# Kernel tuning notes

Hardware: AMD Instinct MI355X
Metric: run time of the kernel (lower is better)

The kernel has to match this reference:

```python
import jax, jax.numpy as jnp
import numpy as np

N_SPK, N_UTT, D = 1024, 32, 128
EPS = 1e-8  # matches F.cosine_similarity eps


def setup_inputs() -> dict:
    key = jax.random.key(0)
    emb = jax.random.normal(key, (N_SPK * N_UTT, D), dtype=jnp.float32)
    emb = emb / jnp.linalg.norm(emb, axis=-1, keepdims=True)  # L2-normalized per docstring
    return {
        "embeddings": emb,
        "w": jnp.asarray(10.0, dtype=jnp.float32),
        "b": jnp.asarray(-5.0, dtype=jnp.float32),
        "n_speakers": N_SPK,
        "n_utterances": N_UTT,
    }


def reference(embeddings, w, b, n_speakers, n_utterances):
    # [N, M, D]
    e = embeddings.reshape(n_speakers, n_utterances, -1)
    cent = e.mean(axis=1)  # [N, D] full centroids
    # exclusive centroids: mean over all utterances except i -> [N, M, D]
    cent_excl = (e.sum(axis=1, keepdims=True) - e) / (n_utterances - 1)

    e_n = jnp.maximum(jnp.linalg.norm(e, axis=-1), EPS)          # [N, M]
    c_n = jnp.maximum(jnp.linalg.norm(cent, axis=-1), EPS)       # [N]
    ce_n = jnp.maximum(jnp.linalg.norm(cent_excl, axis=-1), EPS) # [N, M]

    # cosine sim of every utterance vs every full centroid: [N, M, N]
    sim = jnp.einsum('nmd,kd->nmk', e, cent) / (e_n[:, :, None] * c_n[None, None, :])
    # own-speaker entry uses the exclusive centroid instead
    sim_own = jnp.sum(e * cent_excl, axis=-1) / (e_n * ce_n)     # [N, M]
    eye = jnp.eye(n_speakers, dtype=bool)[:, None, :]            # [N, 1, N]
    sim = jnp.where(eye, sim_own[:, :, None], sim)

    logits = (w * sim + b).reshape(n_speakers * n_utterances, n_speakers)
    targets = jnp.repeat(jnp.arange(n_speakers), n_utterances)
    logp = jax.nn.log_softmax(logits, axis=-1)
    loss = -jnp.take_along_axis(logp, targets[:, None], axis=-1).mean()
    return loss
```

## Files before the change

kernel.cpp:

```cpp
#include <hip/hip_runtime.h>
#include <math.h>

#define NSPK 1024
#define NUTT 32
#define DIM  128
#define NROWS (NSPK * NUTT)
#define EPS 1e-8f
#define LOG2E 1.44269504f

typedef __attribute__((ext_vector_type(8))) short short8;
typedef __attribute__((ext_vector_type(4))) float floatx4;

__device__ inline unsigned short f2bf(float f) {
  union { float f; unsigned u; } v; v.f = f;
  unsigned r = v.u + 0x7fffu + ((v.u >> 16) & 1u);
  return (unsigned short)(r >> 16);
}

__global__ __launch_bounds__(256) void k1(const float* __restrict__ emb,
                                          const float* __restrict__ wp,
                                          const float* __restrict__ bp,
                                          unsigned short* __restrict__ centN,
                                          float* __restrict__ rs2g,
                                          float* __restrict__ eolg,
                                          float* __restrict__ olvg,
                                          float* __restrict__ out) {
  __shared__ __align__(16) float Sl[2 * 128];
  __shared__ float red[4];

  int b = blockIdx.x, t = threadIdx.x;
  float w = wp[0], bb = bp[0];
  float M = bb + fabsf(w);
  if (b == 0 && t == 0) out[0] = 0.f;

  int sp = t >> 7, d = t & 127;
  {
    const float* eb = emb + (size_t)(b * 2 + sp) * NUTT * DIM + d;
    float s = 0.f;
#pragma unroll
    for (int m = 0; m < NUTT; ++m) s += eb[m * DIM];
    Sl[sp * 128 + d] = s;
    float p = s * s;
#pragma unroll
    for (int mask = 1; mask < 64; mask <<= 1) p += __shfl_xor(p, mask, 64);
    if ((t & 63) == 0) red[t >> 6] = p;
  }
  __syncthreads();
  float ss0 = red[0] + red[1], ss1 = red[2] + red[3];

  {
    float ss = sp ? ss1 : ss0;
    float s = Sl[sp * 128 + d];
    float cn = fmaxf(sqrtf(ss) * (1.0f / NUTT), EPS);
    centN[(size_t)(b * 2 + sp) * DIM + d] = f2bf(s / (NUTT * cn));
  }

  {
    int row = t >> 2, sub = t & 3;
    int rsp = row >> 5;
    const float* er = emb + (size_t)(b * 64 + row) * DIM + sub * 32;
    const float* Srow = &Sl[rsp * 128 + sub * 32];
    float ee = 0.f, es = 0.f;
#pragma unroll
    for (int i = 0; i < 8; ++i) {
      float4 ev = *(const float4*)&er[i * 4];
      float4 sv = *(const float4*)&Srow[i * 4];
      ee += ev.x * ev.x + ev.y * ev.y + ev.z * ev.z + ev.w * ev.w;
      es += ev.x * sv.x + ev.y * sv.y + ev.z * sv.z + ev.w * sv.w;
    }
    ee += __shfl_xor(ee, 1, 64); es += __shfl_xor(es, 1, 64);
    ee += __shfl_xor(ee, 2, 64); es += __shfl_xor(es, 2, 64);
    if (sub == 0) {
      float ss = rsp ? ss1 : ss0;
      float en = fmaxf(sqrtf(ee), EPS);
      float dot_own = (es - ee) * (1.0f / (NUTT - 1));
      float ex2 = (ss - 2.f * es + ee) * (1.0f / ((NUTT - 1) * (NUTT - 1)));
      float cen = fmaxf(sqrtf(ex2), EPS);
      float ol = w * dot_own / (en * cen) + bb;
      int gr = b * 64 + row;
      olvg[gr] = ol;
      eolg[gr] = exp2f((ol - M) * LOG2E);
      rs2g[gr] = w * LOG2E / en;
    }
  }
}

__global__ __launch_bounds__(256, 2) void k2(const float* __restrict__ emb,
                                             const unsigned short* __restrict__ centN,
                                             const float* __restrict__ rs2g,
                                             const float* __restrict__ eolg,
                                             const float* __restrict__ olvg,
                                             const float* __restrict__ wp,
                                             const float* __restrict__ bp,
                                             float* __restrict__ out) {
  __shared__ __align__(16) unsigned short A[64 * 136];
  __shared__ __align__(16) unsigned short Bb[2][64 * 136];
  __shared__ __align__(16) float sPart[256];

  int b = blockIdx.x, t = threadIdx.x;
  float w = wp[0], bb = bp[0];
  float M = bb + fabsf(w);
  float c2 = -fabsf(w) * LOG2E;

#pragma unroll
  for (int i = 0; i < 8; ++i) {
    int idx4 = t + 256 * i;
    int r = idx4 >> 5, d4 = (idx4 & 31) << 2;
    float4 v = *(const float4*)(emb + (size_t)b * 8192 + (size_t)idx4 * 4);
    ushort4 bv;
    bv.x = f2bf(v.x); bv.y = f2bf(v.y); bv.z = f2bf(v.z); bv.w = f2bf(v.w);
    *(ushort4*)&A[r * 136 + d4] = bv;
  }
  __syncthreads();

  int wid = t >> 6, lane = t & 63, lg = lane >> 4, lc = lane & 15;

  short8 af[4][4];
#pragma unroll
  for (int rt = 0; rt < 4; ++rt)
#pragma unroll
    for (int ks = 0; ks < 4; ++ks)
      af[rt][ks] = *(const short8*)&A[(rt * 16 + lc) * 136 + ks * 32 + lg * 8];

  float rsL[16], eolL[16];
#pragma unroll
  for (int rt = 0; rt < 4; ++rt) {
    float4 r4 = *(const float4*)&rs2g[b * 64 + rt * 16 + lg * 4];
    float4 o4 = *(const float4*)&eolg[b * 64 + rt * 16 + lg * 4];
    rsL[rt * 4 + 0] = r4.x; rsL[rt * 4 + 1] = r4.y; rsL[rt * 4 + 2] = r4.z; rsL[rt * 4 + 3] = r4.w;
    eolL[rt * 4 + 0] = o4.x; eolL[rt * 4 + 1] = o4.y; eolL[rt * 4 + 2] = o4.z; eolL[rt * 4 + 3] = o4.w;
  }

  float sAcc[16];
#pragma unroll
  for (int j = 0; j < 16; ++j) sAcc[j] = 0.f;

  short8 R[4];
#pragma unroll
  for (int i = 0; i < 4; ++i) {
    int f = t + 256 * i;
    R[i] = *(const short8*)(centN + (size_t)(f >> 4) * DIM + (f & 15) * 8);
  }

  for (int p = 0; p < 16; ++p) {
    unsigned short* Bp = Bb[p & 1];
    __syncthreads();
#pragma unroll
    for (int i = 0; i < 4; ++i) {
      int f = t + 256 * i;
      *(short8*)&Bp[(f >> 4) * 136 + (f & 15) * 8] = R[i];
    }
    {
      int pn = (p + 1) & 15;
#pragma unroll
      for (int i = 0; i < 4; ++i) {
        int f = t + 256 * i;
        R[i] = *(const short8*)(centN + (size_t)(pn * 64 + (f >> 4)) * DIM + (f & 15) * 8);
      }
    }
    __syncthreads();

    short8 bf[4];
#pragma unroll
    for (int ks = 0; ks < 4; ++ks)
      bf[ks] = *(const short8*)&Bp[(wid * 16 + lc) * 136 + ks * 32 + lg * 8];

    floatx4 acc[4];
#pragma unroll
    for (int rt = 0; rt < 4; ++rt) acc[rt] = (floatx4){0.f, 0.f, 0.f, 0.f};
#pragma unroll
    for (int ks = 0; ks < 4; ++ks)
#pragma unroll
      for (int rt = 0; rt < 4; ++rt)
        acc[rt] = __builtin_amdgcn_mfma_f32_16x16x32_bf16(af[rt][ks], bf[ks], acc[rt], 0, 0, 0);

    int col = p * 64 + wid * 16 + lc;
#pragma unroll
    for (int rt = 0; rt < 4; ++rt) {
      int own = b * 2 + (rt >> 1);
      bool isown = (col == own);
#pragma unroll
      for (int reg = 0; reg < 4; ++reg) {
        float l2 = fmaf(rsL[rt * 4 + reg], acc[rt][reg], c2);
        float e = exp2f(l2);
        if (isown) e = eolL[rt * 4 + reg];
        sAcc[rt * 4 + reg] += e;
      }
    }
  }

#pragma unroll
  for (int mask = 1; mask < 16; mask <<= 1)
#pragma unroll
    for (int j = 0; j < 16; ++j) sAcc[j] += __shfl_xor(sAcc[j], mask, 64);

  if (lc == 0)
#pragma unroll
    for (int rt = 0; rt < 4; ++rt)
#pragma unroll
      for (int reg = 0; reg < 4; ++reg)
        sPart[wid * 64 + rt * 16 + lg * 4 + reg] = sAcc[rt * 4 + reg];
  __syncthreads();

  if (t < 64) {
    float st = sPart[t] + sPart[64 + t] + sPart[128 + t] + sPart[192 + t];
    float lossr = M + logf(st) - olvg[b * 64 + t];
#pragma unroll
    for (int mask = 1; mask < 64; mask <<= 1) lossr += __shfl_xor(lossr, mask, 64);
    if (t == 0) atomicAdd(out, lossr * (1.0f / NROWS));
  }
}

extern "C" void kernel_launch(void* const* d_in, const int* in_sizes, int n_in,
                              void* d_out, int out_size, void* d_ws, size_t ws_size,
                              hipStream_t stream) {
  const float* emb = (const float*)d_in[0];
  const float* wp  = (const float*)d_in[1];
  const float* bp  = (const float*)d_in[2];

  char* ws = (char*)d_ws;
  unsigned short* centN = (unsigned short*)ws;
  float* rs2g = (float*)(ws + 262144);
  float* eolg = (float*)(ws + 262144 + 131072);
  float* olvg = (float*)(ws + 262144 + 262144);
  float* out = (float*)d_out;

  hipLaunchKernelGGL(k1, dim3(512), dim3(256), 0, stream,
                     emb, wp, bp, centN, rs2g, eolg, olvg, out);
  hipLaunchKernelGGL(k2, dim3(512), dim3(256), 0, stream,
                     emb, centN, rs2g, eolg, olvg, wp, bp, out);
}
```

Before: 93.81 us.

## Stream centroid tiles straight into LDS with global_load_lds and a chunked layout

k1 now writes the normalized bf16 centroids in a layout grouped into 8-element chunks along the feature dimension. k2 loads each 64-centroid tile with asynchronous global-to-LDS loads (global_load_lds) instead of staging through registers and copying into padded shared memory. Each lane's MFMA B-fragment read becomes one contiguous, conflict-free 16-byte LDS access, and one barrier per iteration is removed. The cost is that correctness now depends on the barrier waiting for the asynchronous LDS writes to finish, and the centroid layout is more specialized.

```diff
diff --git a/kernel.cpp b/kernel.cpp
--- a/kernel.cpp
+++ b/kernel.cpp
@@ -17,10 +17,16 @@
   return (unsigned short)(r >> 16);
 }
 
+__device__ __forceinline__ void gll16(const unsigned short* g, unsigned short* l) {
+  __builtin_amdgcn_global_load_lds(
+      (const __attribute__((address_space(1))) unsigned int*)g,
+      (__attribute__((address_space(3))) unsigned int*)l, 16, 0, 0);
+}
+
 __global__ __launch_bounds__(256) void k1(const float* __restrict__ emb,
                                           const float* __restrict__ wp,
                                           const float* __restrict__ bp,
-                                          unsigned short* __restrict__ centN,
+                                          unsigned short* __restrict__ centC,
                                           float* __restrict__ rs2g,
                                           float* __restrict__ eolg,
                                           float* __restrict__ olvg,
@@ -52,7 +58,8 @@
     float ss = sp ? ss1 : ss0;
     float s = Sl[sp * 128 + d];
     float cn = fmaxf(sqrtf(ss) * (1.0f / NUTT), EPS);
-    centN[(size_t)(b * 2 + sp) * DIM + d] = f2bf(s / (NUTT * cn));
+    centC[(size_t)(d >> 3) * (NSPK * 8) + (size_t)(b * 2 + sp) * 8 + (d & 7)] =
+        f2bf(s / (NUTT * cn));
   }
 
   {
@@ -86,7 +93,7 @@
 }
 
 __global__ __launch_bounds__(256, 2) void k2(const float* __restrict__ emb,
-                                             const unsigned short* __restrict__ centN,
+                                             const unsigned short* __restrict__ centC,
                                              const float* __restrict__ rs2g,
                                              const float* __restrict__ eolg,
                                              const float* __restrict__ olvg,
@@ -94,10 +101,11 @@
                                              const float* __restrict__ bp,
                                              float* __restrict__ out) {
   __shared__ __align__(16) unsigned short A[64 * 136];
-  __shared__ __align__(16) unsigned short Bb[2][64 * 136];
+  __shared__ __align__(16) unsigned short Bb[2][8192];
   __shared__ __align__(16) float sPart[256];
 
   int b = blockIdx.x, t = threadIdx.x;
+  int wid = t >> 6, lane = t & 63, lg = lane >> 4, lc = lane & 15;
   float w = wp[0], bb = bp[0];
   float M = bb + fabsf(w);
   float c2 = -fabsf(w) * LOG2E;
@@ -111,9 +119,15 @@
     bv.x = f2bf(v.x); bv.y = f2bf(v.y); bv.z = f2bf(v.z); bv.w = f2bf(v.w);
     *(ushort4*)&A[r * 136 + d4] = bv;
   }
+
+  const unsigned short* gbase = centC + ((size_t)(wid * 4 + lg) * NSPK + lc) * 8;
+  {
+#pragma unroll
+    for (int i = 0; i < 4; ++i)
+      gll16(gbase + (size_t)i * 16 * 8, &Bb[0][i * 2048 + wid * 512]);
+  }
+
   __syncthreads();
-
-  int wid = t >> 6, lane = t & 63, lg = lane >> 4, lc = lane & 15;
 
   short8 af[4][4];
 #pragma unroll
@@ -135,35 +149,21 @@
 #pragma unroll
   for (int j = 0; j < 16; ++j) sAcc[j] = 0.f;
 
-  short8 R[4];
-#pragma unroll
-  for (int i = 0; i < 4; ++i) {
-    int f = t + 256 * i;
-    R[i] = *(const short8*)(centN + (size_t)(f >> 4) * DIM + (f & 15) * 8);
-  }
-
   for (int p = 0; p < 16; ++p) {
-    unsigned short* Bp = Bb[p & 1];
-    __syncthreads();
-#pragma unroll
-    for (int i = 0; i < 4; ++i) {
-      int f = t + 256 * i;
-      *(short8*)&Bp[(f >> 4) * 136 + (f & 15) * 8] = R[i];
-    }
-    {
-      int pn = (p + 1) & 15;
-#pragma unroll
-      for (int i = 0; i < 4; ++i) {
-        int f = t + 256 * i;
-        R[i] = *(const short8*)(centN + (size_t)(pn * 64 + (f >> 4)) * DIM + (f & 15) * 8);
-      }
-    }
-    __syncthreads();
-
+    if (p > 0) __syncthreads();
+    if (p < 15) {
+      const unsigned short* gp = gbase + (size_t)(p + 1) * 64 * 8;
+      unsigned short* lb = Bb[(p + 1) & 1];
+#pragma unroll
+      for (int i = 0; i < 4; ++i)
+        gll16(gp + (size_t)i * 16 * 8, &lb[i * 2048 + wid * 512]);
+    }
+
+    const unsigned short* Bp = Bb[p & 1];
     short8 bf[4];
 #pragma unroll
     for (int ks = 0; ks < 4; ++ks)
-      bf[ks] = *(const short8*)&Bp[(wid * 16 + lc) * 136 + ks * 32 + lg * 8];
+      bf[ks] = *(const short8*)&Bp[wid * 2048 + ks * 512 + lane * 8];
 
     floatx4 acc[4];
 #pragma unroll
@@ -219,14 +219,14 @@
   const float* bp  = (const float*)d_in[2];
 
   char* ws = (char*)d_ws;
-  unsigned short* centN = (unsigned short*)ws;
+  unsigned short* centC = (unsigned short*)ws;
   float* rs2g = (float*)(ws + 262144);
   float* eolg = (float*)(ws + 262144 + 131072);
   float* olvg = (float*)(ws + 262144 + 262144);
   float* out = (float*)d_out;
 
   hipLaunchKernelGGL(k1, dim3(512), dim3(256), 0, stream,
-                     emb, wp, bp, centN, rs2g, eolg, olvg, out);
+                     emb, wp, bp, centC, rs2g, eolg, olvg, out);
   hipLaunchKernelGGL(k2, dim3(512), dim3(256), 0, stream,
-                     emb, centN, rs2g, eolg, olvg, wp, bp, out);
-}
+                     emb, centC, rs2g, eolg, olvg, wp, bp, out);
+}
```

After: 95.30 us. About the same (+1.6%).
